# Performance work log

Measured on AMD Instinct MI355X. Metric: run time of the kernel, lower is better.

## Reference

```python
import jax, jax.numpy as jnp
import numpy as np

DROPOUT_P = 0.5
HALF_D_LOG_2PI = 8.0  # 0.5 * D * log(2*pi) constant from source, D=16


def _dropout(key, x, p):
    keep = 1.0 - p
    mask = jax.random.bernoulli(key, keep, x.shape).astype(x.dtype)
    return x * mask / keep


def _spmm(adj_vals, row, col, support, n):
    # out[i] = sum_{e: row[e]==i} adj_vals[e] * support[col[e]]
    return jax.ops.segment_sum(adj_vals[:, None] * support[col], row, num_segments=n)


def setup_inputs() -> dict:
    key = jax.random.key(0)
    ks = jax.random.split(key, 9)
    N, F_IN, D, C, E, K = 100000, 512, 16, 16, 3200000, 16
    return {
        "x": jax.random.normal(ks[0], (N, F_IN), dtype=jnp.float32),
        "W1": jax.random.normal(ks[1], (F_IN, D), dtype=jnp.float32) * 0.05,
        "W2": jax.random.normal(ks[2], (D, C), dtype=jnp.float32) * 0.2,
        "adj_vals": jax.random.uniform(ks[3], (E,), dtype=jnp.float32),
        "PI": jax.random.uniform(ks[4], (K,), dtype=jnp.float32, minval=0.01, maxval=1.0),
        "MUs": jax.random.normal(ks[5], (K, D), dtype=jnp.float32),
        "PREs": jax.random.uniform(ks[6], (K, D), dtype=jnp.float32, minval=0.1, maxval=1.0),
        "row": jnp.sort(jax.random.randint(ks[7], (E,), 0, N, dtype=jnp.int32)),
        "col": jax.random.randint(ks[8], (E,), 0, N, dtype=jnp.int32),
    }


def reference(x, W1, W2, adj_vals, PI, MUs, PREs, row, col):
    n = x.shape[0]
    dk1, dk2 = jax.random.split(jax.random.key(42))
    # layer 1: dropout -> linear (P1) -> spmm (P2)
    h = _spmm(adj_vals, row, col, _dropout(dk1, x, DROPOUT_P) @ W1, n)  # [N, D]
    # GMM log-likelihood: log N(h | MU_k, diag(1/PRE_k)) + log PI_k
    diff = h[:, None, :] - MUs[None, :, :]                      # [N, K, D]
    logcomp = (-0.5 * jnp.sum(diff * diff * PREs[None], axis=2)
               + jnp.log(PI)[None, :]
               + 0.5 * jnp.sum(jnp.log(PREs), axis=1)[None, :]
               - HALF_D_LOG_2PI * jnp.log(2.0 * jnp.pi))        # [N, K]
    probs = -jnp.mean(jnp.max(logcomp, axis=1))
    # layer 2: relu -> dropout -> linear -> spmm -> log_softmax
    x1 = jax.nn.relu(h)
    h2 = _spmm(adj_vals, row, col, _dropout(dk2, x1, DROPOUT_P) @ W2, n)  # [N, C]
    return jax.nn.log_softmax(h2, axis=1), probs
```

## Files before the change

kernel.cpp:

```cpp
#include <hip/hip_runtime.h>
#include <stdint.h>

typedef __attribute__((ext_vector_type(8))) short bf16x8;
typedef __attribute__((ext_vector_type(4))) float f32x4;
typedef __attribute__((ext_vector_type(4))) int i32x4;

__host__ __device__ __forceinline__ uint32_t rotl32(uint32_t x, int d){
  return (x << d) | (x >> (32 - d));
}

__host__ __device__ __forceinline__ void threefry2x32(uint32_t k0, uint32_t k1,
                                                      uint32_t x0, uint32_t x1,
                                                      uint32_t* o0, uint32_t* o1){
  uint32_t ks2 = k0 ^ k1 ^ 0x1BD11BDAu;
  x0 += k0; x1 += k1;
  x0 += x1; x1 = rotl32(x1,13); x1 ^= x0;
  x0 += x1; x1 = rotl32(x1,15); x1 ^= x0;
  x0 += x1; x1 = rotl32(x1,26); x1 ^= x0;
  x0 += x1; x1 = rotl32(x1, 6); x1 ^= x0;
  x0 += k1; x1 += ks2 + 1u;
  x0 += x1; x1 = rotl32(x1,17); x1 ^= x0;
  x0 += x1; x1 = rotl32(x1,29); x1 ^= x0;
  x0 += x1; x1 = rotl32(x1,16); x1 ^= x0;
  x0 += x1; x1 = rotl32(x1,24); x1 ^= x0;
  x0 += ks2; x1 += k0 + 2u;
  x0 += x1; x1 = rotl32(x1,13); x1 ^= x0;
  x0 += x1; x1 = rotl32(x1,15); x1 ^= x0;
  x0 += x1; x1 = rotl32(x1,26); x1 ^= x0;
  x0 += x1; x1 = rotl32(x1, 6); x1 ^= x0;
  x0 += k0; x1 += k1 + 3u;
  x0 += x1; x1 = rotl32(x1,17); x1 ^= x0;
  x0 += x1; x1 = rotl32(x1,29); x1 ^= x0;
  x0 += x1; x1 = rotl32(x1,16); x1 ^= x0;
  x0 += x1; x1 = rotl32(x1,24); x1 ^= x0;
  x0 += k1; x1 += ks2 + 4u;
  x0 += x1; x1 = rotl32(x1,13); x1 ^= x0;
  x0 += x1; x1 = rotl32(x1,15); x1 ^= x0;
  x0 += x1; x1 = rotl32(x1,26); x1 ^= x0;
  x0 += x1; x1 = rotl32(x1, 6); x1 ^= x0;
  x0 += ks2; x1 += k0 + 5u;
  *o0 = x0; *o1 = x1;
}

__device__ __forceinline__ uint32_t tf_dropbit(uint32_t k0, uint32_t k1, uint32_t j){
  uint32_t o0, o1;
  threefry2x32(k0, k1, 0u, j, &o0, &o1);
  return (o0 ^ o1) >> 31;
}

__device__ __forceinline__ uint32_t rotl1(uint32_t x, int d){
  return __builtin_amdgcn_alignbit(x, x, (uint32_t)(32 - d));
}

__device__ __forceinline__ ushort f2bf(float f){
  uint32_t u = __float_as_uint(f);
  u += 0x7FFFu + ((u >> 16) & 1u);
  return (ushort)(u >> 16);
}
__device__ __forceinline__ float bf2f(ushort b){
  return __uint_as_float(((uint32_t)b) << 16);
}

__device__ __forceinline__ uint2 drop4(uint32_t k0, uint32_t k1, uint32_t j,
                                       float f0, float f1, float f2, float f3){
  uint32_t ks2 = k0 ^ k1 ^ 0x1BD11BDAu;
  uint32_t xa0 = k0, xa1 = (j + 0u) + k1;
  uint32_t xb0 = k0, xb1 = (j + 1u) + k1;
  uint32_t xc0 = k0, xc1 = (j + 2u) + k1;
  uint32_t xd0 = k0, xd1 = (j + 3u) + k1;
#define RR(d)                                              \
  xa0 += xa1; xa1 = rotl1(xa1, d); xa1 ^= xa0;             \
  xb0 += xb1; xb1 = rotl1(xb1, d); xb1 ^= xb0;             \
  xc0 += xc1; xc1 = rotl1(xc1, d); xc1 ^= xc0;             \
  xd0 += xd1; xd1 = rotl1(xd1, d); xd1 ^= xd0;
#define INJ(ka, kb)                                        \
  { uint32_t A = (ka), B = (kb);                           \
    xa0 += A; xa1 += B; xb0 += A; xb1 += B;                \
    xc0 += A; xc1 += B; xd0 += A; xd1 += B; }
  RR(13) RR(15) RR(26) RR(6)  INJ(k1, ks2 + 1u)
  RR(17) RR(29) RR(16) RR(24) INJ(ks2, k0 + 2u)
  RR(13) RR(15) RR(26) RR(6)  INJ(k0, k1 + 3u)
  RR(17) RR(29) RR(16) RR(24) INJ(k1, ks2 + 4u)
  RR(13) RR(15) RR(26) RR(6)  INJ(ks2, k0 + 5u)
#undef RR
#undef INJ
  uint32_t ba = xa0 ^ xa1, bb = xb0 ^ xb1, bc = xc0 ^ xc1, bd = xd0 ^ xd1;
  uint32_t ua = __float_as_uint(f0) + 0x8000u;
  uint32_t ub = __float_as_uint(f1) + 0x8000u;
  uint32_t uc = __float_as_uint(f2) + 0x8000u;
  uint32_t ud = __float_as_uint(f3) + 0x8000u;
  uint32_t sa = (uint32_t)((int32_t)ba >> 31);
  uint32_t sb = (uint32_t)((int32_t)bb >> 31);
  uint32_t sc = (uint32_t)((int32_t)bc >> 31);
  uint32_t sd = (uint32_t)((int32_t)bd >> 31);
  uint32_t v01 = __builtin_amdgcn_perm(ub, ua, 0x07060302u);
  uint32_t v23 = __builtin_amdgcn_perm(ud, uc, 0x07060302u);
  uint32_t m01 = __builtin_amdgcn_perm(sb, sa, 0x07060302u);
  uint32_t m23 = __builtin_amdgcn_perm(sd, sc, 0x07060302u);
  return make_uint2(v01 & ~m01, v23 & ~m23);
}

__global__ void k_w1pack(const float* __restrict__ W1, ushort* __restrict__ w1p){
  int t = threadIdx.x;
  for (int u = 0; u < 32; ++u){
    int idx = u * 256 + t;
    int k = idx >> 4, c = idx & 15;
    w1p[((k >> 3) * 16 + c) * 8 + (k & 7)] = f2bf(2.0f * W1[idx]);
  }
}

__global__ void k_init(const int* __restrict__ rowv, int* __restrict__ rp,
                       const float* __restrict__ PI, const float* __restrict__ PREs,
                       float* __restrict__ ckg, int N, int E){
  int i = blockIdx.x * 256 + threadIdx.x;
  if (blockIdx.x == 0 && threadIdx.x < 16){
    int k = threadIdx.x;
    float s = logf(PI[k]);
    #pragma unroll
    for (int j = 0; j < 16; ++j) s += 0.5f * logf(PREs[k * 16 + j]);
    ckg[k] = s - 8.0f * logf(6.28318530717958647692f);
  }
  if (i <= N){
    int lo = 0, hi = E;
    while (lo < hi){
      int mid = (lo + hi) >> 1;
      if (rowv[mid] < i) lo = mid + 1; else hi = mid;
    }
    rp[i] = lo;
  }
}

__global__ __launch_bounds__(256, 4) void k_gemm1(
    const float* __restrict__ x, const ushort* __restrict__ w1p,
    ushort* __restrict__ s1, uint32_t dk0, uint32_t dk1, int N){
  __shared__ float part[4][16][17];
  int t = threadIdx.x;
  int l = t & 63, w = t >> 6;
  int rA = l & 15, kg = l >> 4;
  int tb = w >> 1, p = w & 1;
  int r0 = blockIdx.x * 32 + tb * 16;
  int rr = r0 + rA; if (rr > N - 1) rr = N - 1;
  const float4* xv = reinterpret_cast<const float4*>(
      x + (size_t)rr * 512 + (p * 256 + kg * 8));
  uint32_t jb = (uint32_t)rr * 512u + (uint32_t)(p * 256 + kg * 8);

  const bf16x8* bp = reinterpret_cast<const bf16x8*>(w1p);
  bf16x8 Bf[8];
  #pragma unroll
  for (int q = 0; q < 8; ++q) Bf[q] = bp[((p * 8 + q) * 4 + kg) * 16 + rA];

  float4 xa = xv[0], xb = xv[1];
  __builtin_amdgcn_sched_barrier(0);

  f32x4 acc = {0.f, 0.f, 0.f, 0.f};
  #pragma unroll
  for (int ks = 0; ks < 8; ++ks){
    float4 na, nb;
    if (ks < 7){ na = xv[(ks + 1) * 8]; nb = xv[(ks + 1) * 8 + 1]; }
    __builtin_amdgcn_sched_barrier(0);
    uint32_t j0 = jb + (uint32_t)(ks * 32);
    uint2 lo = drop4(dk0, dk1, j0,      xa.x, xa.y, xa.z, xa.w);
    uint2 hi = drop4(dk0, dk1, j0 + 4u, xb.x, xb.y, xb.z, xb.w);
    i32x4 ai = {(int)lo.x, (int)lo.y, (int)hi.x, (int)hi.y};
    bf16x8 a = __builtin_bit_cast(bf16x8, ai);
    acc = __builtin_amdgcn_mfma_f32_16x16x32_bf16(a, Bf[ks], acc, 0, 0, 0);
    if (ks < 7){ xa = na; xb = nb; }
  }

  #pragma unroll
  for (int i2 = 0; i2 < 4; ++i2) part[w][kg * 4 + i2][rA] = acc[i2];
  __syncthreads();
  #pragma unroll
  for (int q = 0; q < 2; ++q){
    int idx = q * 256 + t;
    int tt = idx >> 8, row = (idx >> 4) & 15, col = idx & 15;
    int n = blockIdx.x * 32 + tt * 16 + row;
    float sum = part[tt * 2][row][col] + part[tt * 2 + 1][row][col];
    if (n < N) s1[(size_t)n * 16 + col] = f2bf(sum);
  }
}

__device__ __forceinline__ float edge_sum(const float* __restrict__ adj,
                                          const int* __restrict__ colv,
                                          const ushort* __restrict__ tbl_d,
                                          int e0, int e1){
  float hs = 0.f;
  int e = e0;
  int ea = (e0 + 3) & ~3; if (ea > e1) ea = e1;
  for (; e < ea; ++e) hs += adj[e] * bf2f(tbl_d[(size_t)colv[e] * 16]);
  float a0 = 0.f, a1 = 0.f, a2 = 0.f, a3 = 0.f;
  float b0 = 0.f, b1 = 0.f, b2 = 0.f, b3 = 0.f;
  for (; e + 8 <= e1; e += 8){
    float4 av = *reinterpret_cast<const float4*>(adj + e);
    int4   cv = *reinterpret_cast<const int4*>(colv + e);
    float4 aw = *reinterpret_cast<const float4*>(adj + e + 4);
    int4   cw = *reinterpret_cast<const int4*>(colv + e + 4);
    a0 += av.x * bf2f(tbl_d[(size_t)cv.x * 16]);
    a1 += av.y * bf2f(tbl_d[(size_t)cv.y * 16]);
    a2 += av.z * bf2f(tbl_d[(size_t)cv.z * 16]);
    a3 += av.w * bf2f(tbl_d[(size_t)cv.w * 16]);
    b0 += aw.x * bf2f(tbl_d[(size_t)cw.x * 16]);
    b1 += aw.y * bf2f(tbl_d[(size_t)cw.y * 16]);
    b2 += aw.z * bf2f(tbl_d[(size_t)cw.z * 16]);
    b3 += aw.w * bf2f(tbl_d[(size_t)cw.w * 16]);
  }
  if (e + 4 <= e1){
    float4 av = *reinterpret_cast<const float4*>(adj + e);
    int4   cv = *reinterpret_cast<const int4*>(colv + e);
    a0 += av.x * bf2f(tbl_d[(size_t)cv.x * 16]);
    a1 += av.y * bf2f(tbl_d[(size_t)cv.y * 16]);
    a2 += av.z * bf2f(tbl_d[(size_t)cv.z * 16]);
    a3 += av.w * bf2f(tbl_d[(size_t)cv.w * 16]);
    e += 4;
  }
  for (; e < e1; ++e) hs += adj[e] * bf2f(tbl_d[(size_t)colv[e] * 16]);
  return hs + ((a0 + b0) + (a1 + b1)) + ((a2 + b2) + (a3 + b3));
}

__global__ __launch_bounds__(256) void k_spmm1(
    const float* __restrict__ adj, const int* __restrict__ colv,
    const int* __restrict__ rp, const ushort* __restrict__ s1,
    const float* __restrict__ MUs, const float* __restrict__ PREs,
    const float* __restrict__ W2, const float* __restrict__ ckg,
    ushort* __restrict__ s2, float* __restrict__ partials,
    uint32_t dk0, uint32_t dk1, int N){
  __shared__ float muT[256], preT[256], w2s[256], ck[16];
  __shared__ float bsum;
  int t = threadIdx.x;
  {
    int j = t >> 4, k = t & 15;
    muT[t]  = MUs[k * 16 + j];
    preT[t] = PREs[k * 16 + j];
  }
  w2s[t] = W2[t];
  if (t < 16) ck[t] = ckg[t];
  if (t == 0) bsum = 0.f;
  __syncthreads();

  int i = blockIdx.x * 16 + (t >> 4);
  int d = t & 15;
  int base = t & 48;
  float h = 0.f;
  if (i < N) h = edge_sum(adj, colv, s1 + d, rp[i], rp[i + 1]);

  float lc = ck[d];
  #pragma unroll
  for (int j = 0; j < 16; ++j){
    float hj = __shfl(h, base + j, 64);
    float df = hj - muT[j * 16 + d];
    lc -= 0.5f * df * df * preT[j * 16 + d];
  }
  float m = lc;
  #pragma unroll
  for (int s = 1; s < 16; s <<= 1) m = fmaxf(m, __shfl_xor(m, s, 64));
  float mrow = (d == 0 && i < N) ? m : 0.f;
  mrow += __shfl_xor(mrow, 16, 64);
  mrow += __shfl_xor(mrow, 32, 64);
  if ((t & 63) == 0) atomicAdd(&bsum, mrow);

  float v = fmaxf(h, 0.f);
  float xd2 = (i < N && !tf_dropbit(dk0, dk1, (uint32_t)i * 16u + (uint32_t)d))
              ? 2.0f * v : 0.f;
  float s2v = 0.f;
  #pragma unroll
  for (int j = 0; j < 16; ++j)
    s2v += __shfl(xd2, base + j, 64) * w2s[j * 16 + d];
  if (i < N) s2[(size_t)i * 16 + d] = f2bf(s2v);
  __syncthreads();
  if (t == 0) partials[blockIdx.x] = bsum;
}

__global__ __launch_bounds__(256) void k_spmm2(
    const float* __restrict__ adj, const int* __restrict__ colv,
    const int* __restrict__ rp, const ushort* __restrict__ s2,
    float* __restrict__ out, int N){
  int t = threadIdx.x;
  int i = blockIdx.x * 16 + (t >> 4);
  int d = t & 15;
  float h = 0.f;
  if (i < N) h = edge_sum(adj, colv, s2 + d, rp[i], rp[i + 1]);
  float m = h;
  #pragma unroll
  for (int s = 1; s < 16; s <<= 1) m = fmaxf(m, __shfl_xor(m, s, 64));
  float ex = expf(h - m);
  float ssum = ex;
  #pragma unroll
  for (int s = 1; s < 16; s <<= 1) ssum += __shfl_xor(ssum, s, 64);
  if (i < N) out[(size_t)i * 16 + d] = (h - m) - logf(ssum);
}

__global__ __launch_bounds__(256) void k_fin(const float* __restrict__ partials,
                                             int nparts, float* __restrict__ out, int N){
  __shared__ float wsum[4];
  float s = 0.f;
  for (int i = threadIdx.x; i < nparts; i += 256) s += partials[i];
  #pragma unroll
  for (int sh = 1; sh < 64; sh <<= 1) s += __shfl_xor(s, sh, 64);
  if ((threadIdx.x & 63) == 0) wsum[threadIdx.x >> 6] = s;
  __syncthreads();
  if (threadIdx.x == 0)
    out[(size_t)N * 16] = -(wsum[0] + wsum[1] + wsum[2] + wsum[3]) / (float)N;
}

extern "C" void kernel_launch(void* const* d_in, const int* in_sizes, int n_in,
                              void* d_out, int out_size, void* d_ws, size_t ws_size,
                              hipStream_t stream){
  const float* x    = (const float*)d_in[0];
  const float* W1   = (const float*)d_in[1];
  const float* W2   = (const float*)d_in[2];
  const float* adj  = (const float*)d_in[3];
  const float* PI   = (const float*)d_in[4];
  const float* MUs  = (const float*)d_in[5];
  const float* PREs = (const float*)d_in[6];
  const int*   rowv = (const int*)d_in[7];
  const int*   colv = (const int*)d_in[8];
  const int N = in_sizes[0] / 512;
  const int E = in_sizes[3];
  float* out = (float*)d_out;

  char* ws = (char*)d_ws;
  float* ckg = (float*)ws;
  int*   rp  = (int*)(ws + 256);
  size_t rpBytes = (((size_t)(N + 1) * 4) + 255) & ~(size_t)255;
  ushort* s1 = (ushort*)(ws + 256 + rpBytes);
  size_t s1Bytes = (((size_t)N * 16 * 2) + 255) & ~(size_t)255;
  ushort* s2 = (ushort*)(ws + 256 + rpBytes + s1Bytes);
  size_t s2Bytes = s1Bytes;
  float* partials = (float*)(ws + 256 + rpBytes + s1Bytes + s2Bytes);
  size_t pBytes = ((((size_t)N / 16 + 1) * 4) + 255) & ~(size_t)255;
  ushort* w1p = (ushort*)(ws + 256 + rpBytes + s1Bytes + s2Bytes + pBytes);

  uint32_t d10, d11, d20, d21;
  threefry2x32(0u, 42u, 0u, 0u, &d10, &d11);
  threefry2x32(0u, 42u, 0u, 1u, &d20, &d21);

  int nb0 = (N + 1 + 255) / 256;
  k_init<<<nb0, 256, 0, stream>>>(rowv, rp, PI, PREs, ckg, N, E);
  k_w1pack<<<1, 256, 0, stream>>>(W1, w1p);
  int nb1 = (N + 31) / 32;
  k_gemm1<<<nb1, 256, 0, stream>>>(x, w1p, s1, d10, d11, N);
  int nb2 = (N + 15) / 16;
  k_spmm1<<<nb2, 256, 0, stream>>>(adj, colv, rp, s1, MUs, PREs, W2, ckg,
                                   s2, partials, d20, d21, N);
  k_spmm2<<<nb2, 256, 0, stream>>>(adj, colv, rp, s2, out, N);
  k_fin<<<1, 256, 0, stream>>>(partials, nb2, out, N);
}
```

Baseline: 203.5 us.

## Fuse row-pointer build into GEMM launch and fold tiny kernels together

Replaces the per-row binary-search row-pointer kernel with an edge-parallel boundary scan, and interleaves those blocks with the dropout-GEMM blocks in a single launch (every fifth block runs GEMM). The W1 pack and the log-constant setup merge into one prep kernel, and the final mean reduction moves into block 0 of the second SpMM. The goal is fewer launches and inter-kernel gaps, and letting the memory-bound rowptr scan overlap with GEMM work. In exchange, the grid is heterogeneous and uses modulo block mapping. Block 0 of spmm2 reads partials, which are produced by the previous kernel, so stream ordering keeps that safe.

```diff
diff --git a/kernel.cpp b/kernel.cpp
--- a/kernel.cpp
+++ b/kernel.cpp
@@ -100,45 +100,49 @@
   return make_uint2(v01 & ~m01, v23 & ~m23);
 }
 
-__global__ void k_w1pack(const float* __restrict__ W1, ushort* __restrict__ w1p){
+__global__ void k_prep(const float* __restrict__ W1, ushort* __restrict__ w1p,
+                       const float* __restrict__ PI, const float* __restrict__ PREs,
+                       float* __restrict__ ckg){
   int t = threadIdx.x;
   for (int u = 0; u < 32; ++u){
     int idx = u * 256 + t;
     int k = idx >> 4, c = idx & 15;
     w1p[((k >> 3) * 16 + c) * 8 + (k & 7)] = f2bf(2.0f * W1[idx]);
   }
-}
-
-__global__ void k_init(const int* __restrict__ rowv, int* __restrict__ rp,
-                       const float* __restrict__ PI, const float* __restrict__ PREs,
-                       float* __restrict__ ckg, int N, int E){
-  int i = blockIdx.x * 256 + threadIdx.x;
-  if (blockIdx.x == 0 && threadIdx.x < 16){
-    int k = threadIdx.x;
-    float s = logf(PI[k]);
+  if (t < 16){
+    float s = logf(PI[t]);
     #pragma unroll
-    for (int j = 0; j < 16; ++j) s += 0.5f * logf(PREs[k * 16 + j]);
-    ckg[k] = s - 8.0f * logf(6.28318530717958647692f);
-  }
-  if (i <= N){
-    int lo = 0, hi = E;
-    while (lo < hi){
-      int mid = (lo + hi) >> 1;
-      if (rowv[mid] < i) lo = mid + 1; else hi = mid;
+    for (int j = 0; j < 16; ++j) s += 0.5f * logf(PREs[t * 16 + j]);
+    ckg[t] = s - 8.0f * logf(6.28318530717958647692f);
+  }
+}
+
+__global__ __launch_bounds__(256, 4) void k_main(
+    const float* __restrict__ x, const ushort* __restrict__ w1p,
+    ushort* __restrict__ s1, const int* __restrict__ rowv, int* __restrict__ rp,
+    uint32_t dk0, uint32_t dk1, int N, int E, int nbG, int nbR){
+  __shared__ float part[4][16][17];
+  int bid = blockIdx.x;
+  if (bid % 5 != 0){
+    int rb = bid - bid / 5 - 1;
+    if (rb < nbR){
+      int e = rb * 256 + threadIdx.x;
+      if (e <= E){
+        int r0 = (e > 0) ? rowv[e - 1] : -1;
+        int r1 = (e < E) ? rowv[e] : N;
+        for (int r = r0 + 1; r <= r1; ++r) rp[r] = e;
+      }
     }
-    rp[i] = lo;
-  }
-}
-
-__global__ __launch_bounds__(256, 4) void k_gemm1(
-    const float* __restrict__ x, const ushort* __restrict__ w1p,
-    ushort* __restrict__ s1, uint32_t dk0, uint32_t dk1, int N){
-  __shared__ float part[4][16][17];
+    return;
+  }
+  int gb = bid / 5;
+  if (gb >= nbG) return;
+
   int t = threadIdx.x;
   int l = t & 63, w = t >> 6;
   int rA = l & 15, kg = l >> 4;
   int tb = w >> 1, p = w & 1;
-  int r0 = blockIdx.x * 32 + tb * 16;
+  int r0 = gb * 32 + tb * 16;
   int rr = r0 + rA; if (rr > N - 1) rr = N - 1;
   const float4* xv = reinterpret_cast<const float4*>(
       x + (size_t)rr * 512 + (p * 256 + kg * 8));
@@ -174,7 +178,7 @@
   for (int q = 0; q < 2; ++q){
     int idx = q * 256 + t;
     int tt = idx >> 8, row = (idx >> 4) & 15, col = idx & 15;
-    int n = blockIdx.x * 32 + tt * 16 + row;
+    int n = gb * 32 + tt * 16 + row;
     float sum = part[tt * 2][row][col] + part[tt * 2 + 1][row][col];
     if (n < N) s1[(size_t)n * 16 + col] = f2bf(sum);
   }
@@ -273,6 +277,7 @@
 __global__ __launch_bounds__(256) void k_spmm2(
     const float* __restrict__ adj, const int* __restrict__ colv,
     const int* __restrict__ rp, const ushort* __restrict__ s2,
+    const float* __restrict__ partials, int nparts,
     float* __restrict__ out, int N){
   int t = threadIdx.x;
   int i = blockIdx.x * 16 + (t >> 4);
@@ -287,19 +292,18 @@
   #pragma unroll
   for (int s = 1; s < 16; s <<= 1) ssum += __shfl_xor(ssum, s, 64);
   if (i < N) out[(size_t)i * 16 + d] = (h - m) - logf(ssum);
-}
-
-__global__ __launch_bounds__(256) void k_fin(const float* __restrict__ partials,
-                                             int nparts, float* __restrict__ out, int N){
-  __shared__ float wsum[4];
-  float s = 0.f;
-  for (int i = threadIdx.x; i < nparts; i += 256) s += partials[i];
-  #pragma unroll
-  for (int sh = 1; sh < 64; sh <<= 1) s += __shfl_xor(s, sh, 64);
-  if ((threadIdx.x & 63) == 0) wsum[threadIdx.x >> 6] = s;
-  __syncthreads();
-  if (threadIdx.x == 0)
-    out[(size_t)N * 16] = -(wsum[0] + wsum[1] + wsum[2] + wsum[3]) / (float)N;
+
+  if (blockIdx.x == 0){
+    __shared__ float wsum[4];
+    float s = 0.f;
+    for (int q = t; q < nparts; q += 256) s += partials[q];
+    #pragma unroll
+    for (int sh = 1; sh < 64; sh <<= 1) s += __shfl_xor(s, sh, 64);
+    if ((t & 63) == 0) wsum[t >> 6] = s;
+    __syncthreads();
+    if (t == 0)
+      out[(size_t)N * 16] = -(wsum[0] + wsum[1] + wsum[2] + wsum[3]) / (float)N;
+  }
 }
 
 extern "C" void kernel_launch(void* const* d_in, const int* in_sizes, int n_in,
@@ -334,14 +338,19 @@
   threefry2x32(0u, 42u, 0u, 0u, &d10, &d11);
   threefry2x32(0u, 42u, 0u, 1u, &d20, &d21);
 
-  int nb0 = (N + 1 + 255) / 256;
-  k_init<<<nb0, 256, 0, stream>>>(rowv, rp, PI, PREs, ckg, N, E);
-  k_w1pack<<<1, 256, 0, stream>>>(W1, w1p);
-  int nb1 = (N + 31) / 32;
-  k_gemm1<<<nb1, 256, 0, stream>>>(x, w1p, s1, d10, d11, N);
+  k_prep<<<1, 256, 0, stream>>>(W1, w1p, PI, PREs, ckg);
+
+  int nbG = (N + 31) / 32;
+  int nbR = (E + 1 + 255) / 256;
+  int grid = 5 * nbG + 2;
+  {
+    int maxrb = (grid - 1) - (grid - 1) / 5 - 1;
+    while (maxrb < nbR - 1){ grid += 2; maxrb = (grid - 1) - (grid - 1) / 5 - 1; }
+  }
+  k_main<<<grid, 256, 0, stream>>>(x, w1p, s1, rowv, rp, d10, d11, N, E, nbG, nbR);
+
   int nb2 = (N + 15) / 16;
   k_spmm1<<<nb2, 256, 0, stream>>>(adj, colv, rp, s1, MUs, PREs, W2, ckg,
                                    s2, partials, d20, d21, N);
-  k_spmm2<<<nb2, 256, 0, stream>>>(adj, colv, rp, s2, out, N);
-  k_fin<<<1, 256, 0, stream>>>(partials, nb2, out, N);
-}
+  k_spmm2<<<nb2, 256, 0, stream>>>(adj, colv, rp, s2, partials, nb2, out, N);
+}
```

Result: slower. 208.9 us (+2.7%).
